# Kernel optimization log

Measured on AMD Instinct MI355X. Metric: run time of the kernel, lower is better.

Reference implementation:

```python
import jax, jax.numpy as jnp
import numpy as np

NEG_SLOPE = 0.2  # PyG GATConv default negative_slope
EPS = 1e-16     # PyG softmax denominator epsilon


def gat_layer(x, src, dst, W, att_src, att_dst, bias, N):
    """PyG-style GATConv: gather -> leaky-relu score -> segment softmax -> scatter-add.
    x: [N, F_in], W: [F_in, H*C], att_src/att_dst: [H, C], bias: [H*C].
    src/dst: [E] edge endpoints (messages flow src -> dst), self-loops included.
    """
    H, C = att_src.shape
    h = (x @ W).reshape(N, H, C)                       # [N, H, C]
    a_s = jnp.sum(h * att_src, axis=-1)                # [N, H]
    a_d = jnp.sum(h * att_dst, axis=-1)                # [N, H]
    e = a_s[src] + a_d[dst]                            # [E, H]
    e = jnp.where(e > 0, e, NEG_SLOPE * e)             # leaky relu
    m = jax.ops.segment_max(e, dst, num_segments=N)    # [N, H] (self-loops ensure every node hit)
    p = jnp.exp(e - m[dst])                            # [E, H]
    s = jax.ops.segment_sum(p, dst, num_segments=N)    # [N, H]
    alpha = p / (s[dst] + EPS)                         # [E, H]
    out = jax.ops.segment_sum(alpha[:, :, None] * h[src], dst, num_segments=N)  # [N, H, C]
    return out.reshape(N, H * C) + bias


def setup_inputs() -> dict:
    key = jax.random.key(0)
    ks = jax.random.split(key, 12)
    N, E = 100000, 1600000
    x = jax.random.normal(ks[0], (N, 1), dtype=jnp.float32)
    edge_index = jax.random.randint(ks[1], (2, E), 0, N, dtype=jnp.int32)
    sc = 0.1
    # conv1: in=1, heads=4, out=8
    W1 = jax.random.normal(ks[2], (1, 32), dtype=jnp.float32) * sc
    att_src1 = jax.random.normal(ks[3], (4, 8), dtype=jnp.float32) * sc
    att_dst1 = jax.random.normal(ks[4], (4, 8), dtype=jnp.float32) * sc
    bias1 = jnp.zeros((32,), dtype=jnp.float32)
    # conv2: in=32, heads=8, out=8
    W2 = jax.random.normal(ks[5], (32, 64), dtype=jnp.float32) * sc
    att_src2 = jax.random.normal(ks[6], (8, 8), dtype=jnp.float32) * sc
    att_dst2 = jax.random.normal(ks[7], (8, 8), dtype=jnp.float32) * sc
    bias2 = jnp.zeros((64,), dtype=jnp.float32)
    # fc2: 64 -> 1
    fc_w = jax.random.normal(ks[8], (64, 1), dtype=jnp.float32) * sc
    fc_b = jnp.zeros((1,), dtype=jnp.float32)
    return {"x": x, "edge_index": edge_index,
            "W1": W1, "att_src1": att_src1, "att_dst1": att_dst1, "bias1": bias1,
            "W2": W2, "att_src2": att_src2, "att_dst2": att_dst2, "bias2": bias2,
            "fc_w": fc_w, "fc_b": fc_b}


def reference(x, edge_index, W1, att_src1, att_dst1, bias1,
              W2, att_src2, att_dst2, bias2, fc_w, fc_b):
    N = x.shape[0]
    loop = jnp.arange(N, dtype=edge_index.dtype)       # add_self_loops=True (PyG default)
    src = jnp.concatenate([edge_index[0], loop])
    dst = jnp.concatenate([edge_index[1], loop])
    h = jax.nn.elu(gat_layer(x, src, dst, W1, att_src1, att_dst1, bias1, N))
    h = jax.nn.elu(gat_layer(h, src, dst, W2, att_src2, att_dst2, bias2, N))
    return h @ fc_w + fc_b                             # [N, 1]
```

## Files before the change

kernel.cpp:

```cpp
#include <hip/hip_runtime.h>
#include <hip/hip_fp16.h>
#include <cmath>

#define TPB 256
#define NSLOPE 0.2f
#define SEPS 1e-16f

#define BSH 7
#define BNODES 128
#define NBMAX 1024
#define NCHUNK 512
#define SCTPB 1024
#define SCSTAGE 3360
#define STAGE 2816
#define MAXDEG 96

__device__ __forceinline__ float lrelu(float v) { return v > 0.f ? v : NSLOPE * v; }
__device__ __forceinline__ float elu1(float v)  { return v > 0.f ? v : expm1f(v); }
__device__ __forceinline__ float elu1f(float v) { return v > 0.f ? v : __expf(v) - 1.f; }

__global__ void k_prep(const float* __restrict__ W1, const float* __restrict__ as1,
                       const float* __restrict__ ad1, float* __restrict__ SD,
                       unsigned* __restrict__ bucketCursor, int NB, unsigned cap) {
    int t = threadIdx.x;
    for (int i = t; i < NB; i += blockDim.x) bucketCursor[(size_t)i * 16] = (unsigned)i * cap;
    if (t < 8) {
        int h = t & 3;
        const float* att = (t >= 4) ? ad1 : as1;
        float acc = 0.f;
        #pragma unroll
        for (int c = 0; c < 8; ++c) acc += W1[h*8+c] * att[h*8+c];
        SD[t] = acc;
    }
}

__global__ void k_bscatter(const int* __restrict__ srcI, const int* __restrict__ dstI,
                           int E, int N, int NB, int chunk,
                           unsigned* __restrict__ bucketCursor, int* __restrict__ pk) {
    __shared__ int cnt[NBMAX];
    __shared__ unsigned base[NBMAX];
    __shared__ int offl[NBMAX];
    __shared__ int rval[SCSTAGE];
    __shared__ unsigned short rbkt[SCSTAGE];
    __shared__ int wtot[16], woff[16];
    int t = threadIdx.x;
    int lane = t & 63, wv = t >> 6;
    int ET = E + N;
    int beg = blockIdx.x * chunk;
    int end = min(beg + chunk, ET);
    int m = end - beg;
    for (int i = t; i < NBMAX; i += blockDim.x) cnt[i] = 0;
    __syncthreads();
    for (int e = beg + t; e < end; e += blockDim.x) {
        int d = (e < E) ? dstI[e] : (e - E);
        atomicAdd(&cnt[d >> BSH], 1);
    }
    __syncthreads();
    int v = cnt[t];
    int inc = v;
    #pragma unroll
    for (int off = 1; off < 64; off <<= 1) {
        int u = __shfl_up(inc, off);
        if (lane >= off) inc += u;
    }
    if (lane == 63) wtot[wv] = inc;
    __syncthreads();
    if (t < 16) {
        int xv = wtot[t];
        int sc_ = xv;
        #pragma unroll
        for (int off = 1; off < 16; off <<= 1) {
            int u = __shfl_up(sc_, off);
            if (t >= off) sc_ += u;
        }
        woff[t] = sc_ - xv;
    }
    __syncthreads();
    offl[t] = inc + woff[wv] - v;
    if (t < NB) {
        base[t] = v ? atomicAdd(&bucketCursor[(size_t)t * 16], (unsigned)v) : 0u;
        cnt[t] = 0;
    }
    __syncthreads();
    if (m <= SCSTAGE) {
        for (int e = beg + t; e < end; e += blockDim.x) {
            int s, d;
            if (e < E) { s = srcI[e]; d = dstI[e]; } else { s = d = e - E; }
            int b = d >> BSH;
            int r = atomicAdd(&cnt[b], 1);
            int slot = offl[b] + r;
            rval[slot] = (s << BSH) | (d & (BNODES - 1));
            rbkt[slot] = (unsigned short)b;
        }
        __syncthreads();
        for (int slot = t; slot < m; slot += blockDim.x) {
            int b = rbkt[slot];
            pk[base[b] + (unsigned)(slot - offl[b])] = rval[slot];
        }
    } else {
        for (int e = beg + t; e < end; e += blockDim.x) {
            int s, d;
            if (e < E) { s = srcI[e]; d = dstI[e]; } else { s = d = e - E; }
            int b = d >> BSH;
            int r = atomicAdd(&cnt[b], 1);
            pk[base[b] + (unsigned)r] = (s << BSH) | (d & (BNODES - 1));
        }
    }
}

__global__ void k_sl1h2(const int* __restrict__ pk, const unsigned* __restrict__ bucketCursor,
                        unsigned cap,
                        const float* __restrict__ x, const float* __restrict__ SD,
                        const float* __restrict__ W1, const float* __restrict__ b1,
                        const float* __restrict__ W2, const float* __restrict__ attS,
                        const float* __restrict__ attD, int N,
                        unsigned* __restrict__ offsets, int* __restrict__ sortedSrc,
                        __half* __restrict__ h2h, float* __restrict__ aS, float* __restrict__ aD) {
    __shared__ int sorted[STAGE];
    __shared__ int cnt[BNODES];
    __shared__ int offl[BNODES];
    __shared__ float lds1[BNODES][36];
    int b = blockIdx.x, t = threadIdx.x;
    unsigned rbeg = (unsigned)b * cap;
    int m = (int)(bucketCursor[(size_t)b * 16] - rbeg);
    bool inLds = (m <= STAGE);
    int base = b << BSH;
    if (t < BNODES) cnt[t] = 0;
    __syncthreads();
    for (int i = t; i < m; i += TPB) atomicAdd(&cnt[pk[rbeg + i] & (BNODES - 1)], 1);
    __syncthreads();
    int v = (t < BNODES) ? cnt[t] : 0;
    if (t < BNODES) offl[t] = v;
    __syncthreads();
    for (int off = 1; off < BNODES; off <<= 1) {
        int u = (t >= off && t < BNODES) ? offl[t - off] : 0;
        __syncthreads();
        if (t < BNODES) offl[t] += u;
        __syncthreads();
    }
    if (t < BNODES) {
        int ex = offl[t] - v;
        int d = base + t;
        if (d < N) offsets[d] = ((rbeg + (unsigned)ex) << 10) | (unsigned)v;
        cnt[t] = 0;
        offl[t] = ex;
    }
    __syncthreads();
    if (inLds) {
        for (int i = t; i < m; i += TPB) {
            int p = pk[rbeg + i];
            int dl = p & (BNODES - 1);
            int r = atomicAdd(&cnt[dl], 1);
            sorted[offl[dl] + r] = p >> BSH;
        }
        __syncthreads();
        for (int i = t; i < m; i += TPB) sortedSrc[rbeg + i] = sorted[i];
    } else {
        for (int i = t; i < m; i += TPB) {
            int p = pk[rbeg + i];
            int dl = p & (BNODES - 1);
            int r = atomicAdd(&cnt[dl], 1);
            sortedSrc[rbeg + (unsigned)(offl[dl] + r)] = p >> BSH;
        }
        __syncthreads();
    }
    __syncthreads();
    int n = t >> 1, half = t & 1;
    int d2 = base + n;
    bool active = (d2 < N);
    float s0 = 0.f, s1 = 0.f, s2 = 0.f, s3 = 0.f;
    float g0 = 0.f, g1 = 0.f, g2 = 0.f, g3 = 0.f;
    if (active) {
        int deg = cnt[n];
        int lbeg = offl[n];
        float xd = x[d2];
        float S0 = SD[0], S1 = SD[1], S2 = SD[2], S3 = SD[3];
        float D0 = xd*SD[4], D1 = xd*SD[5], D2 = xd*SD[6], D3 = xd*SD[7];
        int dh = (deg + 1) >> 1;
        int i = lbeg + (half ? dh : 0);
        int rem = half ? (deg - dh) : dh;
        for (; rem >= 2; rem -= 2, i += 2) {
            int a0 = inLds ? sorted[i]   : sortedSrc[rbeg + i];
            int a1 = inLds ? sorted[i+1] : sortedSrc[rbeg + i + 1];
            float x0 = x[a0], x1 = x[a1];
            float p;
            p = __expf(lrelu(x0*S0 + D0)); s0 += p; g0 += p * x0;
            p = __expf(lrelu(x0*S1 + D1)); s1 += p; g1 += p * x0;
            p = __expf(lrelu(x0*S2 + D2)); s2 += p; g2 += p * x0;
            p = __expf(lrelu(x0*S3 + D3)); s3 += p; g3 += p * x0;
            p = __expf(lrelu(x1*S0 + D0)); s0 += p; g0 += p * x1;
            p = __expf(lrelu(x1*S1 + D1)); s1 += p; g1 += p * x1;
            p = __expf(lrelu(x1*S2 + D2)); s2 += p; g2 += p * x1;
            p = __expf(lrelu(x1*S3 + D3)); s3 += p; g3 += p * x1;
        }
        if (rem > 0) {
            int a0 = inLds ? sorted[i] : sortedSrc[rbeg + i];
            float xs = x[a0];
            float p;
            p = __expf(lrelu(xs*S0 + D0)); s0 += p; g0 += p * xs;
            p = __expf(lrelu(xs*S1 + D1)); s1 += p; g1 += p * xs;
            p = __expf(lrelu(xs*S2 + D2)); s2 += p; g2 += p * xs;
            p = __expf(lrelu(xs*S3 + D3)); s3 += p; g3 += p * xs;
        }
    }
    s0 += __shfl_xor(s0, 1); s1 += __shfl_xor(s1, 1);
    s2 += __shfl_xor(s2, 1); s3 += __shfl_xor(s3, 1);
    g0 += __shfl_xor(g0, 1); g1 += __shfl_xor(g1, 1);
    g2 += __shfl_xor(g2, 1); g3 += __shfl_xor(g3, 1);
    if (active) {
        float gg[4];
        gg[0] = g0 / (s0 + SEPS); gg[1] = g1 / (s1 + SEPS);
        gg[2] = g2 / (s2 + SEPS); gg[3] = g3 / (s3 + SEPS);
        int h0 = half * 2;
        #pragma unroll
        for (int hh = 0; hh < 2; ++hh)
            #pragma unroll
            for (int cc = 0; cc < 8; ++cc)
                lds1[n][(h0+hh)*8+cc] = elu1(gg[h0+hh] * W1[(h0+hh)*8+cc] + b1[(h0+hh)*8+cc]);
    }
    __syncthreads();
    int lane = t & 63;
    int sub = t >> 6;
    float w2r[32];
    #pragma unroll
    for (int k = 0; k < 32; ++k) w2r[k] = W2[k*64 + lane];
    float attSl = attS[lane], attDl = attD[lane];
    int nCnt = min(BNODES, N - base);
    for (int nn = sub; nn < nCnt; nn += 4) {
        const float4* row4 = (const float4*)lds1[nn];
        float acc = 0.f;
        #pragma unroll
        for (int k4 = 0; k4 < 8; ++k4) {
            float4 rv = row4[k4];
            acc += rv.x*w2r[4*k4] + rv.y*w2r[4*k4+1] + rv.z*w2r[4*k4+2] + rv.w*w2r[4*k4+3];
        }
        int node = base + nn;
        h2h[(size_t)node*64 + lane] = __float2half(acc);
        float ps = acc * attSl;
        float pd = acc * attDl;
        #pragma unroll
        for (int mm = 1; mm < 8; mm <<= 1) {
            ps += __shfl_xor(ps, mm);
            pd += __shfl_xor(pd, mm);
        }
        int hh = lane >> 3, cc = lane & 7;
        if (cc == 0) aS[(size_t)node*8 + hh] = ps;
        if (cc == 1) aD[(size_t)node*8 + hh] = pd;
    }
}

__global__ void k_agg(const unsigned* __restrict__ offsets, const int* __restrict__ ss,
                      const float* __restrict__ aS, const float* __restrict__ aD,
                      const __half* __restrict__ h2h, const float* __restrict__ b2,
                      const float* __restrict__ fcw, const float* __restrict__ fcb,
                      float* __restrict__ out, int N) {
    __shared__ int sl[4][MAXDEG];
    int lane = threadIdx.x & 63;
    int w = threadIdx.x >> 6;
    int d = blockIdx.x * 4 + w;
    if (d >= N) return;
    unsigned u = offsets[d];
    unsigned beg = u >> 10;
    int deg = (int)(u & 1023u);
    int lH   = lane & 31;
    int half = lane >> 5;
    int hh   = lH >> 2;
    const __half2* __restrict__ hp = (const __half2*)h2h;
    float sum = 0.f, ax = 0.f, ay = 0.f;
    if (deg <= MAXDEG) {
        int degPad = (deg + 7) & ~7;
        for (int j = lane; j < degPad; j += 64) sl[w][j] = ss[beg + (unsigned)min(j, deg - 1)];
        float adv = aD[(unsigned)d * 8u + (unsigned)hh];
        for (int e = 0; e < degPad; e += 8) {
            int bi = e + half;
            int s0 = sl[w][bi],     s1 = sl[w][bi + 2];
            int s2 = sl[w][bi + 4], s3 = sl[w][bi + 6];
            float a0 = aS[(unsigned)s0 * 8u + (unsigned)hh];
            float a1 = aS[(unsigned)s1 * 8u + (unsigned)hh];
            float a2 = aS[(unsigned)s2 * 8u + (unsigned)hh];
            float a3 = aS[(unsigned)s3 * 8u + (unsigned)hh];
            float2 g0 = __half22float2(hp[(unsigned)s0 * 32u + (unsigned)lH]);
            float2 g1 = __half22float2(hp[(unsigned)s1 * 32u + (unsigned)lH]);
            float2 g2 = __half22float2(hp[(unsigned)s2 * 32u + (unsigned)lH]);
            float2 g3 = __half22float2(hp[(unsigned)s3 * 32u + (unsigned)lH]);
            float p0 = __expf(lrelu(a0 + adv));
            float p1 = __expf(lrelu(a1 + adv));
            float p2 = __expf(lrelu(a2 + adv));
            float p3 = __expf(lrelu(a3 + adv));
            if (e + 8 > deg) {
                if (bi     >= deg) p0 = 0.f;
                if (bi + 2 >= deg) p1 = 0.f;
                if (bi + 4 >= deg) p2 = 0.f;
                if (bi + 6 >= deg) p3 = 0.f;
            }
            ax += p0*g0.x + p1*g1.x + p2*g2.x + p3*g3.x;
            ay += p0*g0.y + p1*g1.y + p2*g2.y + p3*g3.y;
            sum += (p0 + p1) + (p2 + p3);
        }
    } else {
        float adh = aD[(size_t)d*8 + hh];
        for (int e = half; e < deg; e += 2) {
            int s = ss[beg + e];
            float p = __expf(lrelu(aS[(size_t)s*8 + hh] + adh));
            float2 g = __half22float2(*(const __half2*)(h2h + (size_t)s*64 + 2*lH));
            ax += p*g.x; ay += p*g.y; sum += p;
        }
    }
    ax  += __shfl_xor(ax, 32);
    ay  += __shfl_xor(ay, 32);
    sum += __shfl_xor(sum, 32);
    float inv = 1.f / (sum + SEPS);
    float tt = elu1f(ax*inv + b2[2*lH]) * fcw[2*lH]
             + elu1f(ay*inv + b2[2*lH+1]) * fcw[2*lH+1];
    #pragma unroll
    for (int m = 16; m; m >>= 1) tt += __shfl_xor(tt, m);
    if (lane == 0) out[d] = tt + fcb[0];
}

extern "C" void kernel_launch(void* const* d_in, const int* in_sizes, int n_in,
                              void* d_out, int out_size, void* d_ws, size_t ws_size,
                              hipStream_t stream) {
    const float* x    = (const float*)d_in[0];
    const int*   ei   = (const int*)  d_in[1];
    const float* W1   = (const float*)d_in[2];
    const float* as1  = (const float*)d_in[3];
    const float* ad1  = (const float*)d_in[4];
    const float* b1   = (const float*)d_in[5];
    const float* W2   = (const float*)d_in[6];
    const float* attS2= (const float*)d_in[7];
    const float* attD2= (const float*)d_in[8];
    const float* b2   = (const float*)d_in[9];
    const float* fcw  = (const float*)d_in[10];
    const float* fcb  = (const float*)d_in[11];
    float* out = (float*)d_out;

    int N = in_sizes[0];
    int E = in_sizes[1] / 2;
    int ET = E + N;
    int NB = (N + BNODES - 1) / BNODES;
    unsigned cap = (unsigned)((ET + NB - 1) / NB + 512);
    cap = (cap + 3u) & ~3u;
    size_t padded = (size_t)NB * cap;

    const int* srcI = ei;
    const int* dstI = ei + E;

    float* ws = (float*)d_ws;
    size_t off = 0;
    float*    SD           = ws + off; off += 16;
    unsigned* bucketCursor = (unsigned*)(ws + off); off += (size_t)NBMAX * 16;
    unsigned* offsets      = (unsigned*)(ws + off); off += (size_t)N + 16;
    int*      pk           = (int*)(ws + off); off += padded;
    int*      sortedSrc    = (int*)(ws + off); off += padded;
    float*    aS2          = ws + off; off += (size_t)N * 8;
    float*    aD2          = ws + off; off += (size_t)N * 8;
    __half*   h2h          = (__half*)(ws + off); off += (size_t)N * 32;

    k_prep<<<1, 1024, 0, stream>>>(W1, as1, ad1, SD, bucketCursor, NB, cap);

    int chunk = (ET + NCHUNK - 1) / NCHUNK;
    k_bscatter<<<NCHUNK, SCTPB, 0, stream>>>(srcI, dstI, E, N, NB, chunk, bucketCursor, pk);
    k_sl1h2   <<<NB, TPB, 0, stream>>>(pk, bucketCursor, cap, x, SD, W1, b1, W2, attS2, attD2,
                                       N, offsets, sortedSrc, h2h, aS2, aD2);
    k_agg     <<<(N + 3) / 4, TPB, 0, stream>>>(offsets, sortedSrc, aS2, aD2, h2h,
                                                b2, fcw, fcb, out, N);
}
```

Before: 204.1 us.

## Software-pipeline layer-2 gather loop and halve scatter chunk size

The layer-2 aggregation loop now prefetches the next group of source indices, attention scores and half-precision features into registers while computing the current group, so the gather latency of one iteration overlaps the arithmetic of the previous one. Separately, the scatter chunk count is halved and the per-block staging size doubled, giving fewer, larger scatter blocks. The prefetch raises register pressure, which may lower occupancy, and the larger staging buffer uses more shared memory per block.

```diff
diff --git a/kernel.cpp b/kernel.cpp
--- a/kernel.cpp
+++ b/kernel.cpp
@@ -9,9 +9,9 @@
 #define BSH 7
 #define BNODES 128
 #define NBMAX 1024
-#define NCHUNK 512
+#define NCHUNK 256
 #define SCTPB 1024
-#define SCSTAGE 3360
+#define SCSTAGE 6720
 #define STAGE 2816
 #define MAXDEG 96
 
@@ -271,31 +271,54 @@
         int degPad = (deg + 7) & ~7;
         for (int j = lane; j < degPad; j += 64) sl[w][j] = ss[beg + (unsigned)min(j, deg - 1)];
         float adv = aD[(unsigned)d * 8u + (unsigned)hh];
+        int bi = half;
+        int s0 = sl[w][bi],     s1 = sl[w][bi + 2];
+        int s2 = sl[w][bi + 4], s3 = sl[w][bi + 6];
+        float a0 = aS[(unsigned)s0 * 8u + (unsigned)hh];
+        float a1 = aS[(unsigned)s1 * 8u + (unsigned)hh];
+        float a2 = aS[(unsigned)s2 * 8u + (unsigned)hh];
+        float a3 = aS[(unsigned)s3 * 8u + (unsigned)hh];
+        float2 g0 = __half22float2(hp[(unsigned)s0 * 32u + (unsigned)lH]);
+        float2 g1 = __half22float2(hp[(unsigned)s1 * 32u + (unsigned)lH]);
+        float2 g2 = __half22float2(hp[(unsigned)s2 * 32u + (unsigned)lH]);
+        float2 g3 = __half22float2(hp[(unsigned)s3 * 32u + (unsigned)lH]);
         for (int e = 0; e < degPad; e += 8) {
-            int bi = e + half;
-            int s0 = sl[w][bi],     s1 = sl[w][bi + 2];
-            int s2 = sl[w][bi + 4], s3 = sl[w][bi + 6];
-            float a0 = aS[(unsigned)s0 * 8u + (unsigned)hh];
-            float a1 = aS[(unsigned)s1 * 8u + (unsigned)hh];
-            float a2 = aS[(unsigned)s2 * 8u + (unsigned)hh];
-            float a3 = aS[(unsigned)s3 * 8u + (unsigned)hh];
-            float2 g0 = __half22float2(hp[(unsigned)s0 * 32u + (unsigned)lH]);
-            float2 g1 = __half22float2(hp[(unsigned)s1 * 32u + (unsigned)lH]);
-            float2 g2 = __half22float2(hp[(unsigned)s2 * 32u + (unsigned)lH]);
-            float2 g3 = __half22float2(hp[(unsigned)s3 * 32u + (unsigned)lH]);
+            bool more = (e + 8) < degPad;
+            int t0, t1, t2, t3;
+            float b0, b1, b2, b3;
+            float2 q0, q1, q2, q3;
+            if (more) {
+                int bj = e + 8 + half;
+                t0 = sl[w][bj];     t1 = sl[w][bj + 2];
+                t2 = sl[w][bj + 4]; t3 = sl[w][bj + 6];
+                b0 = aS[(unsigned)t0 * 8u + (unsigned)hh];
+                b1 = aS[(unsigned)t1 * 8u + (unsigned)hh];
+                b2 = aS[(unsigned)t2 * 8u + (unsigned)hh];
+                b3 = aS[(unsigned)t3 * 8u + (unsigned)hh];
+                q0 = __half22float2(hp[(unsigned)t0 * 32u + (unsigned)lH]);
+                q1 = __half22float2(hp[(unsigned)t1 * 32u + (unsigned)lH]);
+                q2 = __half22float2(hp[(unsigned)t2 * 32u + (unsigned)lH]);
+                q3 = __half22float2(hp[(unsigned)t3 * 32u + (unsigned)lH]);
+            }
             float p0 = __expf(lrelu(a0 + adv));
             float p1 = __expf(lrelu(a1 + adv));
             float p2 = __expf(lrelu(a2 + adv));
             float p3 = __expf(lrelu(a3 + adv));
             if (e + 8 > deg) {
-                if (bi     >= deg) p0 = 0.f;
-                if (bi + 2 >= deg) p1 = 0.f;
-                if (bi + 4 >= deg) p2 = 0.f;
-                if (bi + 6 >= deg) p3 = 0.f;
+                int bc = e + half;
+                if (bc     >= deg) p0 = 0.f;
+                if (bc + 2 >= deg) p1 = 0.f;
+                if (bc + 4 >= deg) p2 = 0.f;
+                if (bc + 6 >= deg) p3 = 0.f;
             }
             ax += p0*g0.x + p1*g1.x + p2*g2.x + p3*g3.x;
             ay += p0*g0.y + p1*g1.y + p2*g2.y + p3*g3.y;
             sum += (p0 + p1) + (p2 + p3);
+            if (more) {
+                s0=t0; s1=t1; s2=t2; s3=t3;
+                a0=b0; a1=b1; a2=b2; a3=b3;
+                g0=q0; g1=q1; g2=q2; g3=q3;
+            }
         }
     } else {
         float adh = aD[(size_t)d*8 + hh];
```

Measured after the change: 196.0 us. -3.9%, faster.

## Pack source attention scores with half features into per-node record; halve scatter chunks

Applied to the files above, without the earlier changes.

Each node's layer-2 fp16 features and its 8 source attention logits now share one 160-byte record, so a gathered edge touches one contiguous region instead of two separate arrays. This aims to cut the number of random cache lines fetched per edge in the aggregation kernel. Separately, the bucket scatter uses half as many chunks with a doubled LDS staging buffer, giving fewer, larger blocks. Records are 160 bytes, which is not a multiple of 128, so some records straddle cache lines.

```diff
diff --git a/kernel.cpp b/kernel.cpp
--- a/kernel.cpp
+++ b/kernel.cpp
@@ -9,11 +9,12 @@
 #define BSH 7
 #define BNODES 128
 #define NBMAX 1024
-#define NCHUNK 512
+#define NCHUNK 256
 #define SCTPB 1024
-#define SCSTAGE 3360
+#define SCSTAGE 6720
 #define STAGE 2816
 #define MAXDEG 96
+#define RECH 80
 
 __device__ __forceinline__ float lrelu(float v) { return v > 0.f ? v : NSLOPE * v; }
 __device__ __forceinline__ float elu1(float v)  { return v > 0.f ? v : expm1f(v); }
@@ -115,7 +116,7 @@
                         const float* __restrict__ W2, const float* __restrict__ attS,
                         const float* __restrict__ attD, int N,
                         unsigned* __restrict__ offsets, int* __restrict__ sortedSrc,
-                        __half* __restrict__ h2h, float* __restrict__ aS, float* __restrict__ aD) {
+                        __half* __restrict__ h2rec, float* __restrict__ aD) {
     __shared__ int sorted[STAGE];
     __shared__ int cnt[BNODES];
     __shared__ int offl[BNODES];
@@ -235,7 +236,8 @@
             acc += rv.x*w2r[4*k4] + rv.y*w2r[4*k4+1] + rv.z*w2r[4*k4+2] + rv.w*w2r[4*k4+3];
         }
         int node = base + nn;
-        h2h[(size_t)node*64 + lane] = __float2half(acc);
+        __half* rec = h2rec + (size_t)node * RECH;
+        rec[lane] = __float2half(acc);
         float ps = acc * attSl;
         float pd = acc * attDl;
         #pragma unroll
@@ -244,14 +246,14 @@
             pd += __shfl_xor(pd, mm);
         }
         int hh = lane >> 3, cc = lane & 7;
-        if (cc == 0) aS[(size_t)node*8 + hh] = ps;
+        if (cc == 0) ((float*)(rec + 64))[hh] = ps;
         if (cc == 1) aD[(size_t)node*8 + hh] = pd;
     }
 }
 
 __global__ void k_agg(const unsigned* __restrict__ offsets, const int* __restrict__ ss,
-                      const float* __restrict__ aS, const float* __restrict__ aD,
-                      const __half* __restrict__ h2h, const float* __restrict__ b2,
+                      const float* __restrict__ aD, const __half* __restrict__ h2rec,
+                      const float* __restrict__ b2,
                       const float* __restrict__ fcw, const float* __restrict__ fcb,
                       float* __restrict__ out, int N) {
     __shared__ int sl[4][MAXDEG];
@@ -265,7 +267,6 @@
     int lH   = lane & 31;
     int half = lane >> 5;
     int hh   = lH >> 2;
-    const __half2* __restrict__ hp = (const __half2*)h2h;
     float sum = 0.f, ax = 0.f, ay = 0.f;
     if (deg <= MAXDEG) {
         int degPad = (deg + 7) & ~7;
@@ -275,14 +276,18 @@
             int bi = e + half;
             int s0 = sl[w][bi],     s1 = sl[w][bi + 2];
             int s2 = sl[w][bi + 4], s3 = sl[w][bi + 6];
-            float a0 = aS[(unsigned)s0 * 8u + (unsigned)hh];
-            float a1 = aS[(unsigned)s1 * 8u + (unsigned)hh];
-            float a2 = aS[(unsigned)s2 * 8u + (unsigned)hh];
-            float a3 = aS[(unsigned)s3 * 8u + (unsigned)hh];
-            float2 g0 = __half22float2(hp[(unsigned)s0 * 32u + (unsigned)lH]);
-            float2 g1 = __half22float2(hp[(unsigned)s1 * 32u + (unsigned)lH]);
-            float2 g2 = __half22float2(hp[(unsigned)s2 * 32u + (unsigned)lH]);
-            float2 g3 = __half22float2(hp[(unsigned)s3 * 32u + (unsigned)lH]);
+            const __half* r0 = h2rec + (size_t)(unsigned)s0 * RECH;
+            const __half* r1 = h2rec + (size_t)(unsigned)s1 * RECH;
+            const __half* r2 = h2rec + (size_t)(unsigned)s2 * RECH;
+            const __half* r3 = h2rec + (size_t)(unsigned)s3 * RECH;
+            float a0 = ((const float*)(r0 + 64))[hh];
+            float a1 = ((const float*)(r1 + 64))[hh];
+            float a2 = ((const float*)(r2 + 64))[hh];
+            float a3 = ((const float*)(r3 + 64))[hh];
+            float2 g0 = __half22float2(((const __half2*)r0)[lH]);
+            float2 g1 = __half22float2(((const __half2*)r1)[lH]);
+            float2 g2 = __half22float2(((const __half2*)r2)[lH]);
+            float2 g3 = __half22float2(((const __half2*)r3)[lH]);
             float p0 = __expf(lrelu(a0 + adv));
             float p1 = __expf(lrelu(a1 + adv));
             float p2 = __expf(lrelu(a2 + adv));
@@ -301,8 +306,9 @@
         float adh = aD[(size_t)d*8 + hh];
         for (int e = half; e < deg; e += 2) {
             int s = ss[beg + e];
-            float p = __expf(lrelu(aS[(size_t)s*8 + hh] + adh));
-            float2 g = __half22float2(*(const __half2*)(h2h + (size_t)s*64 + 2*lH));
+            const __half* r = h2rec + (size_t)(unsigned)s * RECH;
+            float p = __expf(lrelu(((const float*)(r + 64))[hh] + adh));
+            float2 g = __half22float2(((const __half2*)r)[lH]);
             ax += p*g.x; ay += p*g.y; sum += p;
         }
     }
@@ -352,16 +358,15 @@
     unsigned* offsets      = (unsigned*)(ws + off); off += (size_t)N + 16;
     int*      pk           = (int*)(ws + off); off += padded;
     int*      sortedSrc    = (int*)(ws + off); off += padded;
-    float*    aS2          = ws + off; off += (size_t)N * 8;
     float*    aD2          = ws + off; off += (size_t)N * 8;
-    __half*   h2h          = (__half*)(ws + off); off += (size_t)N * 32;
+    __half*   h2rec        = (__half*)(ws + off); off += (size_t)N * 40;
 
     k_prep<<<1, 1024, 0, stream>>>(W1, as1, ad1, SD, bucketCursor, NB, cap);
 
     int chunk = (ET + NCHUNK - 1) / NCHUNK;
     k_bscatter<<<NCHUNK, SCTPB, 0, stream>>>(srcI, dstI, E, N, NB, chunk, bucketCursor, pk);
     k_sl1h2   <<<NB, TPB, 0, stream>>>(pk, bucketCursor, cap, x, SD, W1, b1, W2, attS2, attD2,
-                                       N, offsets, sortedSrc, h2h, aS2, aD2);
-    k_agg     <<<(N + 3) / 4, TPB, 0, stream>>>(offsets, sortedSrc, aS2, aD2, h2h,
+                                       N, offsets, sortedSrc, h2rec, aD2);
+    k_agg     <<<(N + 3) / 4, TPB, 0, stream>>>(offsets, sortedSrc, aD2, h2rec,
                                                 b2, fcw, fcb, out, N);
 }
```

Result: faster. 195.8 us (-4.0%).
